# Kernel tuning notes

Hardware: AMD Instinct MI355X
Metric: run time of the kernel (lower is better)

The kernel has to match this reference:

```python
import jax, jax.numpy as jnp
import numpy as np


def setup_inputs() -> dict:
    key = jax.random.key(0)
    ks = jax.random.split(key, 8)
    B, dz, K, N, dx, T = 64, 16, 16, 1024, 128, 500
    # initial latent state [n_trials, dz, k_particles]
    z0 = jax.random.normal(ks[0], (B, dz, K), jnp.float32)
    # per-latent leak/time-constant A = (1 - dt/tau), kept in (0.8, 0.99) for stability
    A = jax.random.uniform(ks[1], (dz,), jnp.float32, minval=0.8, maxval=0.99)
    # low-rank recurrent factors: n [dz, N] (right), m [N, dz] (left)
    n = jax.random.normal(ks[2], (dz, N), jnp.float32) * (1.0 / N)
    m = jax.random.normal(ks[3], (N, dz), jnp.float32) * (1.0 / np.sqrt(dz))
    # neuron bias h [N], latent bias hz [dz]
    h = jax.random.normal(ks[4], (N,), jnp.float32) * 0.1
    hz = jax.random.normal(ks[5], (dz,), jnp.float32) * 0.01
    # readout B [dz, dx] ~ sqrt(2/dy) randn, bias initialised to zero (as in Observation)
    Bobs = jax.random.normal(ks[6], (dz, dx), jnp.float32) * np.sqrt(2.0 / dz)
    Bias = jnp.zeros((dx,), jnp.float32)
    return {"z0": z0, "A": A, "n": n, "m": m, "h": h, "hz": hz,
            "Bobs": Bobs, "Bias": Bias, "T": T}


def reference(z0, A, n, m, h, hz, Bobs, Bias, T):
    """Low-rank RNN rolled out for T steps + linear (identity-nonlin) readout.

    Per step (Transition.forward with relu nonlinearity, weight_scaler=1, du=0):
        R   = relu(m @ z - h)                       # rates, [B, N, K]
        z'  = A * z + n @ R + hz                    # [B, dz, K]
    Readout (Observation.forward, identity nonlinearity):
        X = einsum('zx,bzTK->bxTK', Bobs, zs) + Bias
    """
    Ab = A[None, :, None]      # [1, dz, 1]
    hb = h[None, :, None]      # [1, N, 1]
    hzb = hz[None, :, None]    # [1, dz, 1]

    def step(z, _):
        X = jnp.einsum('Nz,bzk->bNk', m, z)           # project to neurons
        R = jax.nn.relu(X - hb)                       # rates
        z_new = Ab * z + jnp.einsum('zN,bNk->bzk', n, R) + hzb
        return z_new, z_new

    _, zs = jax.lax.scan(step, z0, None, length=T)    # [T, B, dz, K]
    zs = jnp.transpose(zs, (1, 2, 0, 3))              # [B, dz, T, K]
    # Observation readout
    X = jnp.einsum('zx,bzTK->bxTK', Bobs, zs) + Bias[None, :, None, None]
    return X
```

## Files before the change

### kernel.cpp

```cpp
#include <hip/hip_runtime.h>
#include <hip/hip_bf16.h>


typedef __attribute__((ext_vector_type(4))) short short4v;
typedef __attribute__((ext_vector_type(8))) short short8v;
typedef __attribute__((ext_vector_type(4))) float float4v;

#define BB 64
#define DZ 16
#define KC 16
#define NN 1024
#define DX 128
#define NW 8
#define ITER (NN / (16 * NW))
#define NH (ITER / 2)
#define CH 8

union FragAB {
  short4v s;
  __hip_bfloat162 h2[2];
};
union Frag8 {
  short8v s8;
  short4v s4[2];
};

__device__ inline short4v pack_bf16x4(float a, float b, float c, float d) {
  FragAB u;
  u.h2[0] = __float22bfloat162_rn(make_float2(a, b));
  u.h2[1] = __float22bfloat162_rn(make_float2(c, d));
  return u.s;
}

__device__ inline float4v mfma_bf16(short4v a, short4v b, float4v c) {
#if __has_builtin(__builtin_amdgcn_mfma_f32_16x16x16bf16_1k)
  return __builtin_amdgcn_mfma_f32_16x16x16bf16_1k(a, b, c, 0, 0, 0);
#elif __has_builtin(__builtin_amdgcn_mfma_f32_16x16x16_bf16)
  return __builtin_amdgcn_mfma_f32_16x16x16_bf16(a, b, c, 0, 0, 0);
#else
  float4v d;
  asm("v_mfma_f32_16x16x16_bf16 %0, %1, %2, %3"
      : "=v"(d) : "v"(a), "v"(b), "v"(c));
  return d;
#endif
}

__device__ inline float4v mfma_bf16_x32(short8v a, short8v b, float4v c) {
#if __has_builtin(__builtin_amdgcn_mfma_f32_16x16x32_bf16)
  return __builtin_amdgcn_mfma_f32_16x16x32_bf16(a, b, c, 0, 0, 0);
#else
  float4v d;
  asm("v_mfma_f32_16x16x32_bf16 %0, %1, %2, %3"
      : "=v"(d) : "v"(a), "v"(b), "v"(c));
  return d;
#endif
}

__global__ __launch_bounds__(64 * NW, 2)
void lrrnn_fused(const float* __restrict__ z0, const float* __restrict__ Adec,
                 const float* __restrict__ nmat, const float* __restrict__ mmat,
                 const float* __restrict__ hvec, const float* __restrict__ hzvec,
                 const float* __restrict__ Bobs, const float* __restrict__ Bias,
                 const int* __restrict__ Tptr, float* __restrict__ out)
{
  const int T    = Tptr[0];
  const int b    = blockIdx.x;
  const int tid  = threadIdx.x;
  const int wave = tid >> 6;
  const int lane = tid & 63;
  const int g    = lane >> 4;
  const int c    = lane & 15;

  __shared__ float4v part[2][NW][64];

  FragAB mf[ITER];
  Frag8  nf8[NH];
  float4v negH[ITER];
#pragma unroll
  for (int i = 0; i < ITER; ++i) {
    const int rowbase = wave * (16 * ITER) + i * 16;
    float4v mv = *(const float4v*)(mmat + (rowbase + c) * DZ + g * 4);
    mf[i].s = pack_bf16x4(mv[0], mv[1], mv[2], mv[3]);
    float4v hv = *(const float4v*)(hvec + rowbase + g * 4);
    negH[i][0] = -hv[0]; negH[i][1] = -hv[1];
    negH[i][2] = -hv[2]; negH[i][3] = -hv[3];
  }
#pragma unroll
  for (int i = 0; i < NH; ++i) {
    const int rb0 = wave * (16 * ITER) + (2 * i) * 16;
    float4v nv0 = *(const float4v*)(nmat + c * NN + rb0 + g * 4);
    float4v nv1 = *(const float4v*)(nmat + c * NN + rb0 + 16 + g * 4);
    nf8[i].s4[0] = pack_bf16x4(nv0[0], nv0[1], nv0[2], nv0[3]);
    nf8[i].s4[1] = pack_bf16x4(nv1[0], nv1[1], nv1[2], nv1[3]);
  }

  const float4v Af  = *(const float4v*)(Adec + g * 4);
  const float4v hzf = *(const float4v*)(hzvec + g * 4);
  const float4v zerov = {0.f, 0.f, 0.f, 0.f};

  FragAB bobsF;
  float4v biasF;
  unsigned oof[4];
  {
    const int xb = wave * 16;
    bobsF.s = pack_bf16x4(Bobs[(4 * g + 0) * DX + xb + c],
                          Bobs[(4 * g + 1) * DX + xb + c],
                          Bobs[(4 * g + 2) * DX + xb + c],
                          Bobs[(4 * g + 3) * DX + xb + c]);
    biasF = *(const float4v*)(Bias + xb + g * 4);
#pragma unroll
    for (int rr = 0; rr < 4; ++rr) {
      const int x = xb + g * 4 + rr;
      oof[rr] = (unsigned)(b * DX + x) * (unsigned)T * KC + c;
    }
  }

  float4v zf;
#pragma unroll
  for (int j = 0; j < 4; ++j)
    zf[j] = z0[b * DZ * KC + (g * 4 + j) * KC + c];
  FragAB zb;
  zb.s = pack_bf16x4(zf[0], zf[1], zf[2], zf[3]);

  auto do_step = [&](int buf) {
    float4v az;
#pragma unroll
    for (int j = 0; j < 4; ++j)
      az[j] = fmaf(Af[j], zf[j], hzf[j]);

    float4v xv[ITER];
#pragma unroll
    for (int i = 0; i < ITER; ++i)
      xv[i] = mfma_bf16(mf[i].s, zb.s, negH[i]);

    Frag8 R8[NH];
#pragma unroll
    for (int i = 0; i < NH; ++i) {
      const float4v x0 = xv[2 * i], x1 = xv[2 * i + 1];
      R8[i].s4[0] = pack_bf16x4(fmaxf(x0[0], 0.f), fmaxf(x0[1], 0.f),
                                fmaxf(x0[2], 0.f), fmaxf(x0[3], 0.f));
      R8[i].s4[1] = pack_bf16x4(fmaxf(x1[0], 0.f), fmaxf(x1[1], 0.f),
                                fmaxf(x1[2], 0.f), fmaxf(x1[3], 0.f));
    }

    float4v a0 = mfma_bf16_x32(nf8[0].s8, R8[0].s8, zerov);
    float4v a1 = mfma_bf16_x32(nf8[1].s8, R8[1].s8, zerov);
    a0 = mfma_bf16_x32(nf8[2].s8, R8[2].s8, a0);
    a1 = mfma_bf16_x32(nf8[3].s8, R8[3].s8, a1);

    part[buf][wave][lane] = a0 + a1;
    __syncthreads();

    const float4v p0 = part[buf][0][lane];
    const float4v p1 = part[buf][1][lane];
    const float4v p2 = part[buf][2][lane];
    const float4v p3 = part[buf][3][lane];
    const float4v p4 = part[buf][4][lane];
    const float4v p5 = part[buf][5][lane];
    const float4v p6 = part[buf][6][lane];
    const float4v p7 = part[buf][7][lane];
    const float4v tot = ((p0 + p1) + (p2 + p3)) + ((p4 + p5) + (p6 + p7));
#pragma unroll
    for (int j = 0; j < 4; ++j)
      zf[j] = az[j] + tot[j];
    zb.s = pack_bf16x4(zf[0], zf[1], zf[2], zf[3]);
  };

  int t = 0;
  while (t + CH <= T) {
    short4v hist[CH];
#pragma unroll
    for (int s = 0; s < CH; ++s) {
      do_step(s & 1);
      hist[s] = zb.s;
    }
#pragma unroll
    for (int s = 0; s < CH; ++s) {
      float4v o = mfma_bf16(bobsF.s, hist[s], biasF);
      const unsigned tk = (unsigned)(t + s) * KC;
#pragma unroll
      for (int rr = 0; rr < 4; ++rr)
        out[oof[rr] + tk] = o[rr];
    }
    t += CH;
  }
  for (; t < T; ++t) {
    do_step(t & 1);
    float4v o = mfma_bf16(bobsF.s, zb.s, biasF);
    const unsigned tk = (unsigned)t * KC;
#pragma unroll
    for (int rr = 0; rr < 4; ++rr)
      out[oof[rr] + tk] = o[rr];
  }
}

extern "C" void kernel_launch(void* const* d_in, const int* in_sizes, int n_in,
                              void* d_out, int out_size, void* d_ws, size_t ws_size,
                              hipStream_t stream) {
  const float* z0   = (const float*)d_in[0];
  const float* A    = (const float*)d_in[1];
  const float* nmat = (const float*)d_in[2];
  const float* mmat = (const float*)d_in[3];
  const float* h    = (const float*)d_in[4];
  const float* hz   = (const float*)d_in[5];
  const float* Bobs = (const float*)d_in[6];
  const float* Bias = (const float*)d_in[7];
  const int*   T    = (const int*)d_in[8];
  (void)in_sizes; (void)n_in; (void)out_size; (void)d_ws; (void)ws_size;
  lrrnn_fused<<<dim3(BB), dim3(64 * NW), 0, stream>>>(
      z0, A, nmat, mmat, h, hz, Bobs, Bias, T, (float*)d_out);
}
```

Baseline: 388.6 us.

## Halve waves per block to four, doubling per-wave MFMA work and readout tiles

Each block now runs 4 waves instead of 8, so every wave handles 16 neuron tiles per step and two readout column tiles. The cross-wave reduction through shared memory shrinks from 8 partials to 4, and the per-step barrier synchronises fewer waves. This lengthens each wave's serial MFMA chain per time step and raises register pressure. Launch bounds are relaxed to one block per SIMD group.

```diff
diff --git a/kernel.cpp b/kernel.cpp
--- a/kernel.cpp
+++ b/kernel.cpp
@@ -11,9 +11,10 @@
 #define KC 16
 #define NN 1024
 #define DX 128
-#define NW 8
+#define NW 4
 #define ITER (NN / (16 * NW))
 #define NH (ITER / 2)
+#define NT (DX / (16 * NW))
 #define CH 8
 
 union FragAB {
@@ -56,7 +57,7 @@
 #endif
 }
 
-__global__ __launch_bounds__(64 * NW, 2)
+__global__ __launch_bounds__(64 * NW, 1)
 void lrrnn_fused(const float* __restrict__ z0, const float* __restrict__ Adec,
                  const float* __restrict__ nmat, const float* __restrict__ mmat,
                  const float* __restrict__ hvec, const float* __restrict__ hzvec,
@@ -98,20 +99,21 @@
   const float4v hzf = *(const float4v*)(hzvec + g * 4);
   const float4v zerov = {0.f, 0.f, 0.f, 0.f};
 
-  FragAB bobsF;
-  float4v biasF;
-  unsigned oof[4];
-  {
-    const int xb = wave * 16;
-    bobsF.s = pack_bf16x4(Bobs[(4 * g + 0) * DX + xb + c],
-                          Bobs[(4 * g + 1) * DX + xb + c],
-                          Bobs[(4 * g + 2) * DX + xb + c],
-                          Bobs[(4 * g + 3) * DX + xb + c]);
-    biasF = *(const float4v*)(Bias + xb + g * 4);
+  FragAB bobsF[NT];
+  float4v biasF[NT];
+  unsigned oof[NT][4];
+#pragma unroll
+  for (int s = 0; s < NT; ++s) {
+    const int xb = (wave * NT + s) * 16;
+    bobsF[s].s = pack_bf16x4(Bobs[(4 * g + 0) * DX + xb + c],
+                             Bobs[(4 * g + 1) * DX + xb + c],
+                             Bobs[(4 * g + 2) * DX + xb + c],
+                             Bobs[(4 * g + 3) * DX + xb + c]);
+    biasF[s] = *(const float4v*)(Bias + xb + g * 4);
 #pragma unroll
     for (int rr = 0; rr < 4; ++rr) {
       const int x = xb + g * 4 + rr;
-      oof[rr] = (unsigned)(b * DX + x) * (unsigned)T * KC + c;
+      oof[s][rr] = (unsigned)(b * DX + x) * (unsigned)T * KC + c;
     }
   }
 
@@ -128,38 +130,37 @@
     for (int j = 0; j < 4; ++j)
       az[j] = fmaf(Af[j], zf[j], hzf[j]);
 
-    float4v xv[ITER];
-#pragma unroll
-    for (int i = 0; i < ITER; ++i)
-      xv[i] = mfma_bf16(mf[i].s, zb.s, negH[i]);
-
-    Frag8 R8[NH];
-#pragma unroll
-    for (int i = 0; i < NH; ++i) {
-      const float4v x0 = xv[2 * i], x1 = xv[2 * i + 1];
-      R8[i].s4[0] = pack_bf16x4(fmaxf(x0[0], 0.f), fmaxf(x0[1], 0.f),
-                                fmaxf(x0[2], 0.f), fmaxf(x0[3], 0.f));
-      R8[i].s4[1] = pack_bf16x4(fmaxf(x1[0], 0.f), fmaxf(x1[1], 0.f),
-                                fmaxf(x1[2], 0.f), fmaxf(x1[3], 0.f));
-    }
-
-    float4v a0 = mfma_bf16_x32(nf8[0].s8, R8[0].s8, zerov);
-    float4v a1 = mfma_bf16_x32(nf8[1].s8, R8[1].s8, zerov);
-    a0 = mfma_bf16_x32(nf8[2].s8, R8[2].s8, a0);
-    a1 = mfma_bf16_x32(nf8[3].s8, R8[3].s8, a1);
-
-    part[buf][wave][lane] = a0 + a1;
+    float4v acc[4] = {zerov, zerov, zerov, zerov};
+#pragma unroll
+    for (int grp = 0; grp < 2; ++grp) {
+      float4v xv[8];
+#pragma unroll
+      for (int i = 0; i < 8; ++i)
+        xv[i] = mfma_bf16(mf[grp * 8 + i].s, zb.s, negH[grp * 8 + i]);
+      Frag8 R8[4];
+#pragma unroll
+      for (int i = 0; i < 4; ++i) {
+        const float4v x0 = xv[2 * i], x1 = xv[2 * i + 1];
+        R8[i].s4[0] = pack_bf16x4(fmaxf(x0[0], 0.f), fmaxf(x0[1], 0.f),
+                                  fmaxf(x0[2], 0.f), fmaxf(x0[3], 0.f));
+        R8[i].s4[1] = pack_bf16x4(fmaxf(x1[0], 0.f), fmaxf(x1[1], 0.f),
+                                  fmaxf(x1[2], 0.f), fmaxf(x1[3], 0.f));
+      }
+      acc[grp * 2 + 0] = mfma_bf16_x32(nf8[grp * 4 + 0].s8, R8[0].s8, acc[grp * 2 + 0]);
+      acc[grp * 2 + 1] = mfma_bf16_x32(nf8[grp * 4 + 1].s8, R8[1].s8, acc[grp * 2 + 1]);
+      acc[grp * 2 + 0] = mfma_bf16_x32(nf8[grp * 4 + 2].s8, R8[2].s8, acc[grp * 2 + 0]);
+      acc[grp * 2 + 1] = mfma_bf16_x32(nf8[grp * 4 + 3].s8, R8[3].s8, acc[grp * 2 + 1]);
+    }
+    const float4v zp = (acc[0] + acc[1]) + (acc[2] + acc[3]);
+
+    part[buf][wave][lane] = zp;
     __syncthreads();
 
     const float4v p0 = part[buf][0][lane];
     const float4v p1 = part[buf][1][lane];
     const float4v p2 = part[buf][2][lane];
     const float4v p3 = part[buf][3][lane];
-    const float4v p4 = part[buf][4][lane];
-    const float4v p5 = part[buf][5][lane];
-    const float4v p6 = part[buf][6][lane];
-    const float4v p7 = part[buf][7][lane];
-    const float4v tot = ((p0 + p1) + (p2 + p3)) + ((p4 + p5) + (p6 + p7));
+    const float4v tot = (p0 + p1) + (p2 + p3);
 #pragma unroll
     for (int j = 0; j < 4; ++j)
       zf[j] = az[j] + tot[j];
@@ -176,21 +177,27 @@
     }
 #pragma unroll
     for (int s = 0; s < CH; ++s) {
-      float4v o = mfma_bf16(bobsF.s, hist[s], biasF);
-      const unsigned tk = (unsigned)(t + s) * KC;
-#pragma unroll
-      for (int rr = 0; rr < 4; ++rr)
-        out[oof[rr] + tk] = o[rr];
+#pragma unroll
+      for (int q = 0; q < NT; ++q) {
+        float4v o = mfma_bf16(bobsF[q].s, hist[s], biasF[q]);
+        const unsigned tk = (unsigned)(t + s) * KC;
+#pragma unroll
+        for (int rr = 0; rr < 4; ++rr)
+          out[oof[q][rr] + tk] = o[rr];
+      }
     }
     t += CH;
   }
   for (; t < T; ++t) {
     do_step(t & 1);
-    float4v o = mfma_bf16(bobsF.s, zb.s, biasF);
-    const unsigned tk = (unsigned)t * KC;
-#pragma unroll
-    for (int rr = 0; rr < 4; ++rr)
-      out[oof[rr] + tk] = o[rr];
+#pragma unroll
+    for (int q = 0; q < NT; ++q) {
+      float4v o = mfma_bf16(bobsF[q].s, zb.s, biasF[q]);
+      const unsigned tk = (unsigned)t * KC;
+#pragma unroll
+      for (int rr = 0; rr < 4; ++rr)
+        out[oof[q][rr] + tk] = o[rr];
+    }
   }
 }
 
```

Measured after the change: 393.4 us. No clear change (+1.3%).

## Reduce per-step partials via LDS atomics into triple-buffered accumulator

Applied to the files above, without the earlier changes.

Each wave now adds its 16x16 partial into one shared accumulator with LDS float atomics, replacing the per-wave slots that were summed by an 8-way read after the barrier. A third buffer is cleared one step ahead, so each timestep needs only one barrier. The readout of step t-1 is issued after the barrier of step t to overlap with the next step, and az is computed ahead of time. The cost is 8-way contention on the LDS atomics and a summation order that varies between runs.

```diff
diff --git a/kernel.cpp b/kernel.cpp
--- a/kernel.cpp
+++ b/kernel.cpp
@@ -14,7 +14,8 @@
 #define NW 8
 #define ITER (NN / (16 * NW))
 #define NH (ITER / 2)
-#define CH 8
+
+#define BARRIER_LGKM() asm volatile("s_waitcnt lgkmcnt(0)\n\ts_barrier" ::: "memory")
 
 union FragAB {
   short4v s;
@@ -35,8 +36,6 @@
 __device__ inline float4v mfma_bf16(short4v a, short4v b, float4v c) {
 #if __has_builtin(__builtin_amdgcn_mfma_f32_16x16x16bf16_1k)
   return __builtin_amdgcn_mfma_f32_16x16x16bf16_1k(a, b, c, 0, 0, 0);
-#elif __has_builtin(__builtin_amdgcn_mfma_f32_16x16x16_bf16)
-  return __builtin_amdgcn_mfma_f32_16x16x16_bf16(a, b, c, 0, 0, 0);
 #else
   float4v d;
   asm("v_mfma_f32_16x16x16_bf16 %0, %1, %2, %3"
@@ -71,7 +70,11 @@
   const int g    = lane >> 4;
   const int c    = lane & 15;
 
-  __shared__ float4v part[2][NW][64];
+  __shared__ float4v acc3[3][64];
+
+  if (tid < 3 * 64)
+    acc3[tid >> 6][tid & 63] = (float4v){0.f, 0.f, 0.f, 0.f};
+  __syncthreads();
 
   FragAB mf[ITER];
   Frag8  nf8[NH];
@@ -121,13 +124,13 @@
     zf[j] = z0[b * DZ * KC + (g * 4 + j) * KC + c];
   FragAB zb;
   zb.s = pack_bf16x4(zf[0], zf[1], zf[2], zf[3]);
-
-  auto do_step = [&](int buf) {
-    float4v az;
-#pragma unroll
-    for (int j = 0; j < 4; ++j)
-      az[j] = fmaf(Af[j], zf[j], hzf[j]);
-
+  float4v az;
+#pragma unroll
+  for (int j = 0; j < 4; ++j)
+    az[j] = fmaf(Af[j], zf[j], hzf[j]);
+
+  int buf = 0;
+  for (int t = 0; t < T; ++t) {
     float4v xv[ITER];
 #pragma unroll
     for (int i = 0; i < ITER; ++i)
@@ -147,47 +150,42 @@
     float4v a1 = mfma_bf16_x32(nf8[1].s8, R8[1].s8, zerov);
     a0 = mfma_bf16_x32(nf8[2].s8, R8[2].s8, a0);
     a1 = mfma_bf16_x32(nf8[3].s8, R8[3].s8, a1);
-
-    part[buf][wave][lane] = a0 + a1;
-    __syncthreads();
-
-    const float4v p0 = part[buf][0][lane];
-    const float4v p1 = part[buf][1][lane];
-    const float4v p2 = part[buf][2][lane];
-    const float4v p3 = part[buf][3][lane];
-    const float4v p4 = part[buf][4][lane];
-    const float4v p5 = part[buf][5][lane];
-    const float4v p6 = part[buf][6][lane];
-    const float4v p7 = part[buf][7][lane];
-    const float4v tot = ((p0 + p1) + (p2 + p3)) + ((p4 + p5) + (p6 + p7));
+    const float4v zp = a0 + a1;
+
+    {
+      float* ap = (float*)&acc3[buf][lane];
+      atomicAdd(ap + 0, zp[0]);
+      atomicAdd(ap + 1, zp[1]);
+      atomicAdd(ap + 2, zp[2]);
+      atomicAdd(ap + 3, zp[3]);
+    }
+    BARRIER_LGKM();
+
+    const float4v tot = acc3[buf][lane];
+    const int zbuf_idx = (buf + 2 >= 3) ? buf - 1 : buf + 2;
+    acc3[zbuf_idx][lane] = zerov;
+    if (t > 0) {
+      float4v o = mfma_bf16(bobsF.s, zb.s, biasF);
+      const unsigned tk = (unsigned)(t - 1) * KC;
+#pragma unroll
+      for (int rr = 0; rr < 4; ++rr)
+        out[oof[rr] + tk] = o[rr];
+    }
+
 #pragma unroll
     for (int j = 0; j < 4; ++j)
       zf[j] = az[j] + tot[j];
     zb.s = pack_bf16x4(zf[0], zf[1], zf[2], zf[3]);
-  };
-
-  int t = 0;
-  while (t + CH <= T) {
-    short4v hist[CH];
-#pragma unroll
-    for (int s = 0; s < CH; ++s) {
-      do_step(s & 1);
-      hist[s] = zb.s;
-    }
-#pragma unroll
-    for (int s = 0; s < CH; ++s) {
-      float4v o = mfma_bf16(bobsF.s, hist[s], biasF);
-      const unsigned tk = (unsigned)(t + s) * KC;
-#pragma unroll
-      for (int rr = 0; rr < 4; ++rr)
-        out[oof[rr] + tk] = o[rr];
-    }
-    t += CH;
-  }
-  for (; t < T; ++t) {
-    do_step(t & 1);
+#pragma unroll
+    for (int j = 0; j < 4; ++j)
+      az[j] = fmaf(Af[j], zf[j], hzf[j]);
+
+    buf = (buf + 1 >= 3) ? 0 : buf + 1;
+  }
+
+  {
     float4v o = mfma_bf16(bobsF.s, zb.s, biasF);
-    const unsigned tk = (unsigned)t * KC;
+    const unsigned tk = (unsigned)(T - 1) * KC;
 #pragma unroll
     for (int rr = 0; rr < 4; ++rr)
       out[oof[rr] + tk] = o[rr];
```

Result: slower. 1.485 ms (+282.2%).
